# Optimization experiments

Measured on AMD Instinct MI355X. Metric: run time of the kernel, lower is better.

The kernel has to match this reference:

```python
import jax, jax.numpy as jnp
import numpy as np

SCALE_XY = 10.0  # 1/0.1
SCALE_WH = 5.0   # 1/0.2
GAMMA = 2.0
ALPHA = 0.25
N, C, A = 128, 81, 8732


def setup_inputs() -> dict:
    key = jax.random.key(0)
    ks = jax.random.split(key, 7)
    ploc = jax.random.normal(ks[0], (N, 4, A), jnp.float32)
    plabel = jax.random.normal(ks[1], (N, C, A), jnp.float32)
    # gloc in xywh; wh must be positive for the log() in _loc_vec
    gloc = jax.random.uniform(ks[2], (N, 4, A), jnp.float32, 0.1, 1.0)
    lab = jax.random.randint(ks[3], (N, A), 1, C)
    is_pos = jax.random.uniform(ks[4], (N, A)) < 0.05
    glabel = jnp.where(is_pos, lab, 0).astype(jnp.int32)
    domain_label = jax.random.randint(ks[5], (N,), 0, 2).astype(jnp.int32)
    dboxes = jax.random.uniform(ks[6], (1, 4, A), jnp.float32, 0.1, 1.0)
    return {"ploc": ploc, "plabel": plabel, "gloc": gloc,
            "glabel": glabel, "domain_label": domain_label, "dboxes": dboxes}


def reference(ploc, plabel, gloc, glabel, domain_label, dboxes):
    f32 = ploc.dtype
    mask = glabel > 0                       # [N, A] positives
    pos_num = mask.sum(axis=1)              # [N]

    # _loc_vec: encode ground-truth boxes relative to default boxes
    gxy = SCALE_XY * (gloc[:, :2, :] - dboxes[:, :2, :]) / dboxes[:, 2:, :]
    gwh = SCALE_WH * jnp.log(gloc[:, 2:, :] / dboxes[:, 2:, :])
    vec_gd = jnp.concatenate([gxy, gwh], axis=1)  # [N, 4, A]

    # smooth L1 (beta=1), summed over the 4 coords
    d = ploc - vec_gd
    ad = jnp.abs(d)
    sl1 = jnp.where(ad < 1.0, 0.5 * d * d, ad - 0.5).sum(axis=1)  # [N, A]

    source_mask = (domain_label == 0)[:, None].astype(f32)  # [N, 1]
    sl1 = (source_mask * mask.astype(f32) * sl1).sum(axis=1)  # [N]

    # focal loss per anchor (size_average=False -> elementwise [N, A])
    logp = jax.nn.log_softmax(plabel, axis=1)                 # [N, C, A]
    logpt = jnp.take_along_axis(logp, glabel[:, None, :], axis=1)[:, 0, :]
    pt = jnp.exp(logpt)
    con = -ALPHA * (1.0 - pt) ** GAMMA * logpt                # [N, A]

    # hard negative mining: rank negatives by loss, keep top 3*pos_num
    con_neg = jnp.where(mask, 0.0, con)
    con_idx = jnp.argsort(-con_neg, axis=1)
    con_rank = jnp.argsort(con_idx, axis=1)
    neg_num = jnp.minimum(3 * pos_num, A)[:, None]
    neg_mask = con_rank < neg_num                             # [N, A]

    closs = (con * source_mask * (mask.astype(f32) + neg_mask.astype(f32))).sum(axis=1)

    total_loss = sl1 + closs
    num_mask = (pos_num > 0).astype(f32)
    pn = jnp.clip(pos_num.astype(f32), 1e-6, None)
    return (total_loss * num_mask / pn).mean(axis=0)
```

## Files before the change

### kernel.cpp

```cpp
#include <hip/hip_runtime.h>
#include <math.h>

#define NI 128
#define CC 81
#define AA 8732
#define BX 9

typedef float v4f __attribute__((ext_vector_type(4)));
typedef int   v4i __attribute__((ext_vector_type(4)));


__device__ __forceinline__ void osm_upd(float& m, float& s, float x) {
    float d = x - m;
    float e = __expf(-fabsf(d));
    bool g = d > 0.f;
    s = g ? fmaf(s, e, 1.f) : (s + e);
    m = g ? x : m;
}

__device__ __forceinline__ float sl1f(float d) {
    float ad = fabsf(d);
    return ad < 1.f ? 0.5f * d * d : ad - 0.5f;
}


__global__ __launch_bounds__(256) void k1_focal_loc(
    const float* __restrict__ ploc, const float* __restrict__ plabel,
    const float* __restrict__ gloc, const int* __restrict__ glabel,
    const float* __restrict__ dboxes,
    float* __restrict__ con_out, float* __restrict__ part_sl1,
    float* __restrict__ part_poscon, int* __restrict__ part_posnum)
{
    const int n  = blockIdx.y;
    const int t4 = blockIdx.x * blockDim.x + threadIdx.x;
    const int a  = t4 * 4;

    float slm = 0.f, poscon = 0.f;
    int poscnt = 0;

    if (a < AA) {
        const v4i gl = *(const v4i*)(glabel + (size_t)n * AA + a);

        float m0=-3e38f, m1=-3e38f, m2=-3e38f, m3=-3e38f;
        float s0=0.f, s1=0.f, s2=0.f, s3=0.f;
        float x0=0.f, x1=0.f, x2=0.f, x3=0.f;
        const float* pb = plabel + (size_t)n * CC * AA + a;
        #pragma unroll 3
        for (int c = 0; c < CC; ++c) {
            v4f x = __builtin_nontemporal_load((const v4f*)(pb + (size_t)c * AA));
            if (c == gl.x) x0 = x.x;
            if (c == gl.y) x1 = x.y;
            if (c == gl.z) x2 = x.z;
            if (c == gl.w) x3 = x.w;
            osm_upd(m0, s0, x.x);
            osm_upd(m1, s1, x.y);
            osm_upd(m2, s2, x.z);
            osm_upd(m3, s3, x.w);
        }
        float lp0 = x0 - m0 - __logf(s0);
        float lp1 = x1 - m1 - __logf(s1);
        float lp2 = x2 - m2 - __logf(s2);
        float lp3 = x3 - m3 - __logf(s3);
        float pt0 = __expf(lp0), pt1 = __expf(lp1), pt2 = __expf(lp2), pt3 = __expf(lp3);
        float o0 = 1.f - pt0, o1 = 1.f - pt1, o2 = 1.f - pt2, o3 = 1.f - pt3;
        float c0 = -0.25f * o0 * o0 * lp0;
        float c1 = -0.25f * o1 * o1 * lp1;
        float c2 = -0.25f * o2 * o2 * lp2;
        float c3 = -0.25f * o3 * o3 * lp3;

        v4f cv; cv.x = c0; cv.y = c1; cv.z = c2; cv.w = c3;
        __builtin_nontemporal_store(cv, (v4f*)(con_out + (size_t)n * AA + a));

        const v4f dbx = *(const v4f*)(dboxes + 0 * AA + a);
        const v4f dby = *(const v4f*)(dboxes + 1 * AA + a);
        const v4f dbw = *(const v4f*)(dboxes + 2 * AA + a);
        const v4f dbh = *(const v4f*)(dboxes + 3 * AA + a);
        const float* gb = gloc + (size_t)n * 4 * AA + a;
        const v4f gx = __builtin_nontemporal_load((const v4f*)(gb + 0 * AA));
        const v4f gy = __builtin_nontemporal_load((const v4f*)(gb + 1 * AA));
        const v4f gw = __builtin_nontemporal_load((const v4f*)(gb + 2 * AA));
        const v4f gh = __builtin_nontemporal_load((const v4f*)(gb + 3 * AA));
        const float* pp = ploc + (size_t)n * 4 * AA + a;
        const v4f px = __builtin_nontemporal_load((const v4f*)(pp + 0 * AA));
        const v4f py = __builtin_nontemporal_load((const v4f*)(pp + 1 * AA));
        const v4f pw = __builtin_nontemporal_load((const v4f*)(pp + 2 * AA));
        const v4f ph = __builtin_nontemporal_load((const v4f*)(pp + 3 * AA));

        #define LOC1(j) ( sl1f(px.j - 10.f * (gx.j - dbx.j) / dbw.j) \
                        + sl1f(py.j - 10.f * (gy.j - dby.j) / dbh.j) \
                        + sl1f(pw.j - 5.f * __logf(gw.j / dbw.j))    \
                        + sl1f(ph.j - 5.f * __logf(gh.j / dbh.j)) )
        float l0 = LOC1(x), l1 = LOC1(y), l2 = LOC1(z), l3 = LOC1(w);
        #undef LOC1

        if (gl.x > 0) { slm += l0; poscon += c0; poscnt++; }
        if (gl.y > 0) { slm += l1; poscon += c1; poscnt++; }
        if (gl.z > 0) { slm += l2; poscon += c2; poscnt++; }
        if (gl.w > 0) { slm += l3; poscon += c3; poscnt++; }
    }

    for (int off = 32; off; off >>= 1) {
        slm    += __shfl_down(slm, off);
        poscon += __shfl_down(poscon, off);
        poscnt += __shfl_down(poscnt, off);
    }
    __shared__ float rs[4], rp[4];
    __shared__ int   rc[4];
    const int wid = threadIdx.x >> 6, lane = threadIdx.x & 63;
    if (lane == 0) { rs[wid] = slm; rp[wid] = poscon; rc[wid] = poscnt; }
    __syncthreads();
    if (threadIdx.x == 0) {
        const int slot = n * BX + blockIdx.x;
        part_sl1[slot]    = rs[0] + rs[1] + rs[2] + rs[3];
        part_poscon[slot] = rp[0] + rp[1] + rp[2] + rp[3];
        part_posnum[slot] = rc[0] + rc[1] + rc[2] + rc[3];
    }
}


__global__ __launch_bounds__(256) void k2_select(
    const float* __restrict__ con, const int* __restrict__ glabel,
    const int* __restrict__ domain,
    const float* __restrict__ part_sl1, const float* __restrict__ part_poscon,
    const int* __restrict__ part_posnum,
    float* __restrict__ img_total)
{
    const int n = blockIdx.x;
    const int tid = threadIdx.x;
    __shared__ float cn[AA];
    __shared__ float redf[4];
    __shared__ int   redi[4];
    __shared__ float s_sl1, s_pc;
    __shared__ int   s_pos;

    if (tid == 0) {
        float a = 0.f, b = 0.f; int c = 0;
        #pragma unroll
        for (int j = 0; j < BX; ++j) {
            a += part_sl1[n * BX + j];
            b += part_poscon[n * BX + j];
            c += part_posnum[n * BX + j];
        }
        s_sl1 = a; s_pc = b; s_pos = c;
    }
    for (int i = tid; i < AA; i += 256) {
        float c = con[(size_t)n * AA + i];
        cn[i] = (glabel[(size_t)n * AA + i] > 0) ? 0.f : c;
    }
    __syncthreads();

    const int pos = s_pos;
    const int dom = domain[n];
    float total = 0.f;

    if (dom == 0 && pos > 0) {
        const int K = min(3 * pos, AA);

        unsigned lo = 0u, hi = 0x7f800000u;
        while (lo < hi) {
            unsigned mid = lo + (hi - lo + 1u) / 2u;
            const float mv = __uint_as_float(mid);
            int cnt = 0;
            for (int i = tid; i < AA; i += 256) cnt += (cn[i] >= mv);
            for (int off = 32; off; off >>= 1) cnt += __shfl_down(cnt, off);
            if ((tid & 63) == 0) redi[tid >> 6] = cnt;
            __syncthreads();
            cnt = redi[0] + redi[1] + redi[2] + redi[3];
            __syncthreads();
            if (cnt >= K) lo = mid; else hi = mid - 1u;
        }
        const float tval = __uint_as_float(lo);

        int cgt = 0; float sgt = 0.f;
        for (int i = tid; i < AA; i += 256) {
            float v = cn[i];
            if (v > tval) { cgt++; sgt += v; }
        }
        for (int off = 32; off; off >>= 1) {
            cgt += __shfl_down(cgt, off);
            sgt += __shfl_down(sgt, off);
        }
        if ((tid & 63) == 0) { redi[tid >> 6] = cgt; redf[tid >> 6] = sgt; }
        __syncthreads();
        cgt = redi[0] + redi[1] + redi[2] + redi[3];
        sgt = redf[0] + redf[1] + redf[2] + redf[3];

        const float closs_neg = sgt + (float)(K - cgt) * tval;
        total = (s_sl1 + s_pc + closs_neg) / (float)pos;
    }

    if (tid == 0) img_total[n] = total;
}


__global__ __launch_bounds__(128) void k3_final(
    const float* __restrict__ img_total, float* __restrict__ out)
{
    const int tid = threadIdx.x;
    float v = img_total[tid];
    for (int off = 32; off; off >>= 1) v += __shfl_down(v, off);
    __shared__ float r[2];
    if ((tid & 63) == 0) r[tid >> 6] = v;
    __syncthreads();
    if (tid == 0) out[0] = (r[0] + r[1]) / (float)NI;
}


extern "C" void kernel_launch(void* const* d_in, const int* in_sizes, int n_in,
                              void* d_out, int out_size, void* d_ws, size_t ws_size,
                              hipStream_t stream)
{
    const float* ploc   = (const float*)d_in[0];
    const float* plabel = (const float*)d_in[1];
    const float* gloc   = (const float*)d_in[2];
    const int*   glabel = (const int*)d_in[3];
    const int*   domain = (const int*)d_in[4];
    const float* dboxes = (const float*)d_in[5];

    float* con         = (float*)d_ws;
    float* part_sl1    = con + (size_t)NI * AA;
    float* part_poscon = part_sl1 + NI * BX;
    int*   part_posnum = (int*)(part_poscon + NI * BX);
    float* img_total   = (float*)(part_posnum + NI * BX);

    dim3 g1(BX, NI);
    k1_focal_loc<<<g1, 256, 0, stream>>>(ploc, plabel, gloc, glabel, dboxes,
                                         con, part_sl1, part_poscon, part_posnum);
    k2_select<<<NI, 256, 0, stream>>>(con, glabel, domain,
                                      part_sl1, part_poscon, part_posnum, img_total);
    k3_final<<<1, 128, 0, stream>>>(img_total, (float*)d_out);
}
```

Measured before the change: 508.6 us.

## Keep selection values in registers, fold final reduction into atomics, drop nontemporal hints

```diff
diff --git a/kernel.cpp b/kernel.cpp
--- a/kernel.cpp
+++ b/kernel.cpp
@@ -5,6 +5,7 @@
 #define CC 81
 #define AA 8732
 #define BX 9
+#define VPT 35
 
 typedef float v4f __attribute__((ext_vector_type(4)));
 typedef int   v4i __attribute__((ext_vector_type(4)));
@@ -29,11 +30,14 @@
     const float* __restrict__ gloc, const int* __restrict__ glabel,
     const float* __restrict__ dboxes,
     float* __restrict__ con_out, float* __restrict__ part_sl1,
-    float* __restrict__ part_poscon, int* __restrict__ part_posnum)
+    float* __restrict__ part_poscon, int* __restrict__ part_posnum,
+    float* __restrict__ out)
 {
     const int n  = blockIdx.y;
     const int t4 = blockIdx.x * blockDim.x + threadIdx.x;
     const int a  = t4 * 4;
+
+    if (blockIdx.x == 0 && blockIdx.y == 0 && threadIdx.x == 0) out[0] = 0.f;
 
     float slm = 0.f, poscon = 0.f;
     int poscnt = 0;
@@ -47,7 +51,7 @@
         const float* pb = plabel + (size_t)n * CC * AA + a;
         #pragma unroll 3
         for (int c = 0; c < CC; ++c) {
-            v4f x = __builtin_nontemporal_load((const v4f*)(pb + (size_t)c * AA));
+            v4f x = *(const v4f*)(pb + (size_t)c * AA);
             if (c == gl.x) x0 = x.x;
             if (c == gl.y) x1 = x.y;
             if (c == gl.z) x2 = x.z;
@@ -69,22 +73,22 @@
         float c3 = -0.25f * o3 * o3 * lp3;
 
         v4f cv; cv.x = c0; cv.y = c1; cv.z = c2; cv.w = c3;
-        __builtin_nontemporal_store(cv, (v4f*)(con_out + (size_t)n * AA + a));
+        *(v4f*)(con_out + (size_t)n * AA + a) = cv;
 
         const v4f dbx = *(const v4f*)(dboxes + 0 * AA + a);
         const v4f dby = *(const v4f*)(dboxes + 1 * AA + a);
         const v4f dbw = *(const v4f*)(dboxes + 2 * AA + a);
         const v4f dbh = *(const v4f*)(dboxes + 3 * AA + a);
         const float* gb = gloc + (size_t)n * 4 * AA + a;
-        const v4f gx = __builtin_nontemporal_load((const v4f*)(gb + 0 * AA));
-        const v4f gy = __builtin_nontemporal_load((const v4f*)(gb + 1 * AA));
-        const v4f gw = __builtin_nontemporal_load((const v4f*)(gb + 2 * AA));
-        const v4f gh = __builtin_nontemporal_load((const v4f*)(gb + 3 * AA));
+        const v4f gx = *(const v4f*)(gb + 0 * AA);
+        const v4f gy = *(const v4f*)(gb + 1 * AA);
+        const v4f gw = *(const v4f*)(gb + 2 * AA);
+        const v4f gh = *(const v4f*)(gb + 3 * AA);
         const float* pp = ploc + (size_t)n * 4 * AA + a;
-        const v4f px = __builtin_nontemporal_load((const v4f*)(pp + 0 * AA));
-        const v4f py = __builtin_nontemporal_load((const v4f*)(pp + 1 * AA));
-        const v4f pw = __builtin_nontemporal_load((const v4f*)(pp + 2 * AA));
-        const v4f ph = __builtin_nontemporal_load((const v4f*)(pp + 3 * AA));
+        const v4f px = *(const v4f*)(pp + 0 * AA);
+        const v4f py = *(const v4f*)(pp + 1 * AA);
+        const v4f pw = *(const v4f*)(pp + 2 * AA);
+        const v4f ph = *(const v4f*)(pp + 3 * AA);
 
         #define LOC1(j) ( sl1f(px.j - 10.f * (gx.j - dbx.j) / dbw.j) \
                         + sl1f(py.j - 10.f * (gy.j - dby.j) / dbh.j) \
@@ -123,86 +127,74 @@
     const int* __restrict__ domain,
     const float* __restrict__ part_sl1, const float* __restrict__ part_poscon,
     const int* __restrict__ part_posnum,
-    float* __restrict__ img_total)
+    float* __restrict__ out)
 {
     const int n = blockIdx.x;
     const int tid = threadIdx.x;
-    __shared__ float cn[AA];
     __shared__ float redf[4];
     __shared__ int   redi[4];
-    __shared__ float s_sl1, s_pc;
-    __shared__ int   s_pos;
+
+    if (domain[n] != 0) return;
+    int pos = 0;
+    #pragma unroll
+    for (int j = 0; j < BX; ++j) pos += part_posnum[n * BX + j];
+    if (pos == 0) return;
+    const int K = min(3 * pos, AA);
+
+    float vals[VPT];
+    #pragma unroll
+    for (int j = 0; j < VPT; ++j) {
+        const int i = tid + j * 256;
+        float v = 0.f;
+        if (i < AA) {
+            float c = con[(size_t)n * AA + i];
+            v = (glabel[(size_t)n * AA + i] > 0) ? 0.f : c;
+        }
+        vals[j] = v;
+    }
+
+    unsigned lo = 0u, hi = 0x7f800000u;
+    while (lo < hi) {
+        unsigned mid = lo + (hi - lo + 1u) / 2u;
+        const float mv = __uint_as_float(mid);
+        int cnt = 0;
+        #pragma unroll
+        for (int j = 0; j < VPT; ++j) cnt += (vals[j] >= mv);
+        for (int off = 32; off; off >>= 1) cnt += __shfl_down(cnt, off);
+        if ((tid & 63) == 0) redi[tid >> 6] = cnt;
+        __syncthreads();
+        cnt = redi[0] + redi[1] + redi[2] + redi[3];
+        __syncthreads();
+        if (cnt >= K) lo = mid; else hi = mid - 1u;
+    }
+    const float tval = __uint_as_float(lo);
+
+    int cgt = 0; float sgt = 0.f;
+    #pragma unroll
+    for (int j = 0; j < VPT; ++j) {
+        float v = vals[j];
+        if (v > tval) { cgt++; sgt += v; }
+    }
+    for (int off = 32; off; off >>= 1) {
+        cgt += __shfl_down(cgt, off);
+        sgt += __shfl_down(sgt, off);
+    }
+    if ((tid & 63) == 0) { redi[tid >> 6] = cgt; redf[tid >> 6] = sgt; }
+    __syncthreads();
 
     if (tid == 0) {
-        float a = 0.f, b = 0.f; int c = 0;
+        const int   tcgt = redi[0] + redi[1] + redi[2] + redi[3];
+        const float tsgt = redf[0] + redf[1] + redf[2] + redf[3];
+        float sl1 = 0.f, pc = 0.f;
         #pragma unroll
         for (int j = 0; j < BX; ++j) {
-            a += part_sl1[n * BX + j];
-            b += part_poscon[n * BX + j];
-            c += part_posnum[n * BX + j];
+            sl1 += part_sl1[n * BX + j];
+            pc  += part_poscon[n * BX + j];
         }
-        s_sl1 = a; s_pc = b; s_pos = c;
-    }
-    for (int i = tid; i < AA; i += 256) {
-        float c = con[(size_t)n * AA + i];
-        cn[i] = (glabel[(size_t)n * AA + i] > 0) ? 0.f : c;
-    }
-    __syncthreads();
-
-    const int pos = s_pos;
-    const int dom = domain[n];
-    float total = 0.f;
-
-    if (dom == 0 && pos > 0) {
-        const int K = min(3 * pos, AA);
-
-        unsigned lo = 0u, hi = 0x7f800000u;
-        while (lo < hi) {
-            unsigned mid = lo + (hi - lo + 1u) / 2u;
-            const float mv = __uint_as_float(mid);
-            int cnt = 0;
-            for (int i = tid; i < AA; i += 256) cnt += (cn[i] >= mv);
-            for (int off = 32; off; off >>= 1) cnt += __shfl_down(cnt, off);
-            if ((tid & 63) == 0) redi[tid >> 6] = cnt;
-            __syncthreads();
-            cnt = redi[0] + redi[1] + redi[2] + redi[3];
-            __syncthreads();
-            if (cnt >= K) lo = mid; else hi = mid - 1u;
-        }
-        const float tval = __uint_as_float(lo);
-
-        int cgt = 0; float sgt = 0.f;
-        for (int i = tid; i < AA; i += 256) {
-            float v = cn[i];
-            if (v > tval) { cgt++; sgt += v; }
-        }
-        for (int off = 32; off; off >>= 1) {
-            cgt += __shfl_down(cgt, off);
-            sgt += __shfl_down(sgt, off);
-        }
-        if ((tid & 63) == 0) { redi[tid >> 6] = cgt; redf[tid >> 6] = sgt; }
-        __syncthreads();
-        cgt = redi[0] + redi[1] + redi[2] + redi[3];
-        sgt = redf[0] + redf[1] + redf[2] + redf[3];
-
-        const float closs_neg = sgt + (float)(K - cgt) * tval;
-        total = (s_sl1 + s_pc + closs_neg) / (float)pos;
-    }
-
-    if (tid == 0) img_total[n] = total;
-}
-
-
-__global__ __launch_bounds__(128) void k3_final(
-    const float* __restrict__ img_total, float* __restrict__ out)
-{
-    const int tid = threadIdx.x;
-    float v = img_total[tid];
-    for (int off = 32; off; off >>= 1) v += __shfl_down(v, off);
-    __shared__ float r[2];
-    if ((tid & 63) == 0) r[tid >> 6] = v;
-    __syncthreads();
-    if (tid == 0) out[0] = (r[0] + r[1]) / (float)NI;
+        const float closs_neg = tsgt + (float)(K - tcgt) * tval;
+        const float total = (sl1 + pc + closs_neg) / (float)pos;
+        atomicAdd(out, total * (1.f / (float)NI));
+    }
 }
 
 
@@ -216,17 +208,16 @@
     const int*   glabel = (const int*)d_in[3];
     const int*   domain = (const int*)d_in[4];
     const float* dboxes = (const float*)d_in[5];
+    float* out = (float*)d_out;
 
     float* con         = (float*)d_ws;
     float* part_sl1    = con + (size_t)NI * AA;
     float* part_poscon = part_sl1 + NI * BX;
     int*   part_posnum = (int*)(part_poscon + NI * BX);
-    float* img_total   = (float*)(part_posnum + NI * BX);
 
     dim3 g1(BX, NI);
     k1_focal_loc<<<g1, 256, 0, stream>>>(ploc, plabel, gloc, glabel, dboxes,
-                                         con, part_sl1, part_poscon, part_posnum);
+                                         con, part_sl1, part_poscon, part_posnum, out);
     k2_select<<<NI, 256, 0, stream>>>(con, glabel, domain,
-                                      part_sl1, part_poscon, part_posnum, img_total);
-    k3_final<<<1, 128, 0, stream>>>(img_total, (float*)d_out);
-}
+                                      part_sl1, part_poscon, part_posnum, out);
+}
```

Result: slower. 531.8 us (+4.6%).
